# Optimization experiments

Hardware: AMD Instinct MI355X
Metric: run time of the kernel (lower is better)

## Reference

```python
import math
import jax, jax.numpy as jnp
import numpy as np

HEADS = 16
MASKED_BIAS = -10000.0


def setup_inputs() -> dict:
    key = jax.random.key(0)
    kq, kk, kv = jax.random.split(key, 3)
    B, S, D = 4, 1024, 2048
    q = jax.random.normal(kq, (B, S, D), dtype=jnp.float32)
    k = jax.random.normal(kk, (B, S, D), dtype=jnp.float32)
    v = jax.random.normal(kv, (B, S, D), dtype=jnp.float32)
    return {"q": q, "k": k, "v": v}


def _mha(q, k, v):
    B, Sq, D = q.shape
    Sk = k.shape[-2]
    hd = D // HEADS
    # (B, H, S, hd)
    qh = q.reshape(B, Sq, HEADS, hd).transpose(0, 2, 1, 3)
    kh = k.reshape(B, Sk, HEADS, hd).transpose(0, 2, 1, 3)
    vh = v.reshape(B, Sk, HEADS, hd).transpose(0, 2, 1, 3)
    scores = jnp.einsum("bhqd,bhkd->bhqk", qh, kh) / math.sqrt(hd)
    # causal mask: query i attends to keys <= i (aligned to end of kv)
    qi = jnp.arange(Sq)[:, None] + (Sk - Sq)
    ki = jnp.arange(Sk)[None, :]
    causal = ki <= qi  # (Sq, Sk)
    scores = jnp.where(causal[None, None], scores, jnp.asarray(MASKED_BIAS, scores.dtype))
    attn = jax.nn.softmax(scores, axis=-1)
    out = jnp.einsum("bhqk,bhkd->bhqd", attn, vh)
    return out.transpose(0, 2, 1, 3).reshape(B, Sq, D)


def reference(q, k, v):
    return _mha(q, k, v)
```

## Files before the change

### kernel.cpp

```cpp
#include <hip/hip_runtime.h>
#include <hip/hip_bf16.h>


#define HEADS  16
#define HD     128
#define SEQ    1024
#define DMODEL 2048

typedef _Float16 f16;
typedef __attribute__((ext_vector_type(8))) _Float16 f16x8;
typedef __attribute__((ext_vector_type(4))) _Float16 f16x4;
typedef __attribute__((ext_vector_type(4))) float    f32x4;
typedef __attribute__((ext_vector_type(4))) unsigned int u32x4;

__device__ __forceinline__ unsigned int pkrtz(float a, float b) {
    return __builtin_bit_cast(unsigned int, __builtin_amdgcn_cvt_pkrtz(a, b));
}

__global__ __launch_bounds__(256, 2)
void fa_fwd(const float* __restrict__ Q,
            const float* __restrict__ K,
            const float* __restrict__ V,
            float* __restrict__ O)
{
    __shared__ f16 kT[2][64 * 128];
    __shared__ f16 vT[2][128 * 64];

    const int tid  = threadIdx.x;
    const int lane = tid & 63;
    const int wv   = tid >> 6;
    const int quad = lane >> 4;
    const int cl   = lane & 15;

    const int bh = blockIdx.x;
    const int qt = 15 - blockIdx.y;
    const int qb = qt * 64;
    const long long head_off = ((long long)(bh >> 4) * SEQ) * DMODEL
                             + (long long)(bh & 15) * HD;
    const float rscale = 0.08838834764831845f;

    const int krow = tid >> 4;
    const int kg   = tid & 15;
    const int kgs  = kg ^ krow;
    const int vr0  = (tid & 31) * 2;
    const int vcg  = tid >> 5;
    const int vg   = vr0 >> 3;
    const int vo   = vr0 & 7;

    f32x4 kraw[8], vraw[8];

    auto loadKV = [&](int kbase) {
        #pragma unroll
        for (int i = 0; i < 4; ++i) {
            const float* kp = K + head_off + (long long)(kbase + krow + i * 16) * DMODEL + kg * 8;
            kraw[2 * i]     = *(const f32x4*)kp;
            kraw[2 * i + 1] = *(const f32x4*)(kp + 4);
        }
        const float* vp = V + head_off + (long long)(kbase + vr0) * DMODEL + vcg * 16;
        #pragma unroll
        for (int j = 0; j < 4; ++j) {
            vraw[j]     = *(const f32x4*)(vp + 4 * j);
            vraw[4 + j] = *(const f32x4*)(vp + DMODEL + 4 * j);
        }
    };

    auto stageKV = [&](int buf) {
        #pragma unroll
        for (int i = 0; i < 4; ++i) {
            u32x4 w;
            w.x = pkrtz(kraw[2 * i][0], kraw[2 * i][1]);
            w.y = pkrtz(kraw[2 * i][2], kraw[2 * i][3]);
            w.z = pkrtz(kraw[2 * i + 1][0], kraw[2 * i + 1][1]);
            w.w = pkrtz(kraw[2 * i + 1][2], kraw[2 * i + 1][3]);
            *(u32x4*)&kT[buf][(krow + 16 * i) * 128 + kgs * 8] = w;
        }
        #pragma unroll
        for (int j = 0; j < 16; ++j) {
            unsigned int pk = pkrtz(vraw[j >> 2][j & 3], vraw[4 + (j >> 2)][j & 3]);
            *(unsigned int*)&vT[buf][(vcg * 16 + j) * 64 + ((vg ^ (j & 7)) * 8) + vo] = pk;
        }
    };

    const int qrow = qb + wv * 16 + cl;
    f16x8 qf[4];
    {
        const float* qp = Q + head_off + (long long)qrow * DMODEL + quad * 8;
        #pragma unroll
        for (int kk = 0; kk < 4; ++kk) {
            f32x4 qa = *(const f32x4*)(qp + kk * 32);
            f32x4 qc = *(const f32x4*)(qp + kk * 32 + 4);
            union { f16x8 v; unsigned int u[4]; } qw;
            qw.u[0] = pkrtz(qa[0], qa[1]);
            qw.u[1] = pkrtz(qa[2], qa[3]);
            qw.u[2] = pkrtz(qc[0], qc[1]);
            qw.u[3] = pkrtz(qc[2], qc[3]);
            qf[kk] = qw.v;
        }
    }

    f32x4 acc[8];
    #pragma unroll
    for (int i = 0; i < 8; ++i) acc[i] = (f32x4){0.f, 0.f, 0.f, 0.f};
    float ls = 0.f;

    loadKV(0);
    stageKV(0);
    __syncthreads();

    #pragma unroll 1
    for (int kt = 0; kt <= qt; ++kt) {
        const int c = kt & 1;

        if (kt < qt) loadKV((kt + 1) * 64);

        f32x4 sc[4];
        #pragma unroll
        for (int st = 0; st < 4; ++st) sc[st] = (f32x4){0.f, 0.f, 0.f, 0.f};
        __builtin_amdgcn_s_setprio(1);
        #pragma unroll
        for (int kk = 0; kk < 4; ++kk) {
            #pragma unroll
            for (int st = 0; st < 4; ++st) {
                f16x8 kf = *(const f16x8*)&kT[c][(st * 16 + cl) * 128
                                               + ((kk * 4 + quad) ^ cl) * 8];
                sc[st] = __builtin_amdgcn_mfma_f32_16x16x32_f16(kf, qf[kk], sc[st], 0, 0, 0);
            }
        }
        __builtin_amdgcn_s_setprio(0);

        if (kt < qt) stageKV(c ^ 1);

        const int kbase = kt * 64;
        f16x4 pf[4];
        if (kt == qt) {
            #pragma unroll
            for (int st = 0; st < 4; ++st) {
                float e[4];
                #pragma unroll
                for (int r = 0; r < 4; ++r) {
                    int key = kbase + st * 16 + quad * 4 + r;
                    float ex = __expf(sc[st][r] * rscale);
                    e[r] = (key <= qrow) ? ex : 0.f;
                    ls += e[r];
                }
                union { f16x4 v; unsigned int u[2]; } pw;
                pw.u[0] = pkrtz(e[0], e[1]);
                pw.u[1] = pkrtz(e[2], e[3]);
                pf[st] = pw.v;
            }
        } else {
            #pragma unroll
            for (int st = 0; st < 4; ++st) {
                float e[4];
                #pragma unroll
                for (int r = 0; r < 4; ++r) {
                    e[r] = __expf(sc[st][r] * rscale);
                    ls += e[r];
                }
                union { f16x4 v; unsigned int u[2]; } pw;
                pw.u[0] = pkrtz(e[0], e[1]);
                pw.u[1] = pkrtz(e[2], e[3]);
                pf[st] = pw.v;
            }
        }

        __builtin_amdgcn_s_setprio(1);
        #pragma unroll
        for (int dt = 0; dt < 8; ++dt) {
            #pragma unroll
            for (int st = 0; st < 4; ++st) {
                f16x4 vf = *(const f16x4*)&vT[c][(dt * 16 + cl) * 64
                                                + ((st * 2 + (quad >> 1)) ^ (cl & 7)) * 8
                                                + (quad & 1) * 4];
                acc[dt] = __builtin_amdgcn_mfma_f32_16x16x16f16(vf, pf[st], acc[dt], 0, 0, 0);
            }
        }
        __builtin_amdgcn_s_setprio(0);

        if (kt < qt) __syncthreads();
    }

    float lsum = ls;
    lsum += __shfl_xor(lsum, 16, 64);
    lsum += __shfl_xor(lsum, 32, 64);
    const float rl = 1.0f / lsum;

    float* op = O + head_off + (long long)qrow * DMODEL + quad * 4;
    #pragma unroll
    for (int dt = 0; dt < 8; ++dt) {
        f32x4 o4 = acc[dt];
        o4[0] *= rl; o4[1] *= rl; o4[2] *= rl; o4[3] *= rl;
        *(f32x4*)(op + dt * 16) = o4;
    }
}

extern "C" void kernel_launch(void* const* d_in, const int* in_sizes, int n_in,
                              void* d_out, int out_size, void* d_ws, size_t ws_size,
                              hipStream_t stream) {
    const float* q = (const float*)d_in[0];
    const float* k = (const float*)d_in[1];
    const float* v = (const float*)d_in[2];
    float* o = (float*)d_out;

    dim3 grid(4 * HEADS, SEQ / 64);
    dim3 block(256);
    fa_fwd<<<grid, block, 0, stream>>>(q, k, v, o);
}
```

Baseline: 170.5 us.

## Pre-convert K/V to swizzled fp16 image and DMA tiles directly into LDS

Adds a prep kernel that converts each 64-key K/V tile from fp32 to fp16 in the attention kernel's swizzled LDS layout and stores it in a global scratch image. The attention kernel then fills LDS with global_load_lds DMA copies instead of loading fp32 into registers, converting and storing to LDS on every reuse. This aims to halve the global bytes re-read per tile and free registers and ALU work in the main loop. The trade-off is an extra kernel launch, an extra pass over K/V, and reliance on the barrier to wait for the asynchronous LDS DMA to complete.

```diff
diff --git a/kernel.cpp b/kernel.cpp
--- a/kernel.cpp
+++ b/kernel.cpp
@@ -6,6 +6,7 @@
 #define HD     128
 #define SEQ    1024
 #define DMODEL 2048
+#define IMG_CHUNK 32768
 
 typedef _Float16 f16;
 typedef __attribute__((ext_vector_type(8))) _Float16 f16x8;
@@ -13,15 +14,77 @@
 typedef __attribute__((ext_vector_type(4))) float    f32x4;
 typedef __attribute__((ext_vector_type(4))) unsigned int u32x4;
 
+typedef __attribute__((address_space(1))) const unsigned char gl_u8;
+typedef __attribute__((address_space(3))) unsigned char lds_u8;
+
+__device__ unsigned char KVIMG[64ull * 16ull * IMG_CHUNK];
+
 __device__ __forceinline__ unsigned int pkrtz(float a, float b) {
     return __builtin_bit_cast(unsigned int, __builtin_amdgcn_cvt_pkrtz(a, b));
 }
 
+__device__ __forceinline__ void dma16(const void* g, void* l) {
+    __builtin_amdgcn_global_load_lds((gl_u8*)g, (lds_u8*)l, 16, 0, 0);
+}
+
 __global__ __launch_bounds__(256, 2)
-void fa_fwd(const float* __restrict__ Q,
-            const float* __restrict__ K,
-            const float* __restrict__ V,
-            float* __restrict__ O)
+void prep_kv(const float* __restrict__ K, const float* __restrict__ V)
+{
+    __shared__ f16 kL[64 * 128];
+    __shared__ f16 vL[128 * 64];
+
+    const int tid = threadIdx.x;
+    const int bh  = blockIdx.x;
+    const int kb  = blockIdx.y;
+    const long long head_off = ((long long)(bh >> 4) * SEQ) * DMODEL
+                             + (long long)(bh & 15) * HD;
+    const int kbase = kb * 64;
+
+    const int krow = tid >> 4;
+    const int kg   = tid & 15;
+    const int kgs  = kg ^ krow;
+    #pragma unroll
+    for (int i = 0; i < 4; ++i) {
+        const float* kp = K + head_off + (long long)(kbase + krow + 16 * i) * DMODEL + kg * 8;
+        f32x4 a = *(const f32x4*)kp;
+        f32x4 b = *(const f32x4*)(kp + 4);
+        u32x4 w;
+        w.x = pkrtz(a[0], a[1]); w.y = pkrtz(a[2], a[3]);
+        w.z = pkrtz(b[0], b[1]); w.w = pkrtz(b[2], b[3]);
+        *(u32x4*)&kL[(krow + 16 * i) * 128 + kgs * 8] = w;
+    }
+    const int vr0 = (tid & 31) * 2;
+    const int vcg = tid >> 5;
+    const int vg  = vr0 >> 3;
+    const int vo  = vr0 & 7;
+    {
+        const float* vp = V + head_off + (long long)(kbase + vr0) * DMODEL + vcg * 16;
+        f32x4 va[4], vb[4];
+        #pragma unroll
+        for (int j = 0; j < 4; ++j) {
+            va[j] = *(const f32x4*)(vp + 4 * j);
+            vb[j] = *(const f32x4*)(vp + DMODEL + 4 * j);
+        }
+        #pragma unroll
+        for (int j = 0; j < 16; ++j) {
+            unsigned int pk = pkrtz(va[j >> 2][j & 3], vb[j >> 2][j & 3]);
+            *(unsigned int*)&vL[(vcg * 16 + j) * 64 + ((vg ^ (j & 7)) * 8) + vo] = pk;
+        }
+    }
+    __syncthreads();
+
+    unsigned char* dst = KVIMG + ((long long)(bh * 16 + kb)) * IMG_CHUNK;
+    const unsigned char* ks = (const unsigned char*)kL;
+    const unsigned char* vs = (const unsigned char*)vL;
+    #pragma unroll
+    for (int i = 0; i < 4; ++i) {
+        *(u32x4*)(dst + tid * 16 + i * 4096)         = *(const u32x4*)(ks + tid * 16 + i * 4096);
+        *(u32x4*)(dst + 16384 + tid * 16 + i * 4096) = *(const u32x4*)(vs + tid * 16 + i * 4096);
+    }
+}
+
+__global__ __launch_bounds__(256, 2)
+void fa_fwd(const float* __restrict__ Q, float* __restrict__ O)
 {
     __shared__ f16 kT[2][64 * 128];
     __shared__ f16 vT[2][128 * 64];
@@ -39,46 +102,16 @@
                              + (long long)(bh & 15) * HD;
     const float rscale = 0.08838834764831845f;
 
-    const int krow = tid >> 4;
-    const int kg   = tid & 15;
-    const int kgs  = kg ^ krow;
-    const int vr0  = (tid & 31) * 2;
-    const int vcg  = tid >> 5;
-    const int vg   = vr0 >> 3;
-    const int vo   = vr0 & 7;
-
-    f32x4 kraw[8], vraw[8];
-
-    auto loadKV = [&](int kbase) {
-        #pragma unroll
-        for (int i = 0; i < 4; ++i) {
-            const float* kp = K + head_off + (long long)(kbase + krow + i * 16) * DMODEL + kg * 8;
-            kraw[2 * i]     = *(const f32x4*)kp;
-            kraw[2 * i + 1] = *(const f32x4*)(kp + 4);
-        }
-        const float* vp = V + head_off + (long long)(kbase + vr0) * DMODEL + vcg * 16;
-        #pragma unroll
-        for (int j = 0; j < 4; ++j) {
-            vraw[j]     = *(const f32x4*)(vp + 4 * j);
-            vraw[4 + j] = *(const f32x4*)(vp + DMODEL + 4 * j);
-        }
-    };
-
-    auto stageKV = [&](int buf) {
-        #pragma unroll
-        for (int i = 0; i < 4; ++i) {
-            u32x4 w;
-            w.x = pkrtz(kraw[2 * i][0], kraw[2 * i][1]);
-            w.y = pkrtz(kraw[2 * i][2], kraw[2 * i][3]);
-            w.z = pkrtz(kraw[2 * i + 1][0], kraw[2 * i + 1][1]);
-            w.w = pkrtz(kraw[2 * i + 1][2], kraw[2 * i + 1][3]);
-            *(u32x4*)&kT[buf][(krow + 16 * i) * 128 + kgs * 8] = w;
-        }
-        #pragma unroll
-        for (int j = 0; j < 16; ++j) {
-            unsigned int pk = pkrtz(vraw[j >> 2][j & 3], vraw[4 + (j >> 2)][j & 3]);
-            *(unsigned int*)&vT[buf][(vcg * 16 + j) * 64 + ((vg ^ (j & 7)) * 8) + vo] = pk;
-        }
+    const unsigned char* img = KVIMG + (long long)bh * 16 * IMG_CHUNK;
+
+    auto issueTile = [&](int buf, int kt) {
+        const unsigned char* src = img + (long long)kt * IMG_CHUNK + wv * 4096 + lane * 16;
+        unsigned char* kb = (unsigned char*)&kT[buf][0] + wv * 4096;
+        unsigned char* vb = (unsigned char*)&vT[buf][0] + wv * 4096;
+        #pragma unroll
+        for (int i = 0; i < 4; ++i) dma16(src + i * 1024,          kb + i * 1024);
+        #pragma unroll
+        for (int i = 0; i < 4; ++i) dma16(src + 16384 + i * 1024,  vb + i * 1024);
     };
 
     const int qrow = qb + wv * 16 + cl;
@@ -103,15 +136,15 @@
     for (int i = 0; i < 8; ++i) acc[i] = (f32x4){0.f, 0.f, 0.f, 0.f};
     float ls = 0.f;
 
-    loadKV(0);
-    stageKV(0);
-    __syncthreads();
+    issueTile(0, 0);
 
     #pragma unroll 1
     for (int kt = 0; kt <= qt; ++kt) {
         const int c = kt & 1;
 
-        if (kt < qt) loadKV((kt + 1) * 64);
+        __syncthreads();
+
+        if (kt < qt) issueTile(c ^ 1, kt + 1);
 
         f32x4 sc[4];
         #pragma unroll
@@ -127,8 +160,6 @@
             }
         }
         __builtin_amdgcn_s_setprio(0);
-
-        if (kt < qt) stageKV(c ^ 1);
 
         const int kbase = kt * 64;
         f16x4 pf[4];
@@ -176,8 +207,6 @@
             }
         }
         __builtin_amdgcn_s_setprio(0);
-
-        if (kt < qt) __syncthreads();
     }
 
     float lsum = ls;
@@ -202,7 +231,6 @@
     const float* v = (const float*)d_in[2];
     float* o = (float*)d_out;
 
-    dim3 grid(4 * HEADS, SEQ / 64);
-    dim3 block(256);
-    fa_fwd<<<grid, block, 0, stream>>>(q, k, v, o);
-}
+    prep_kv<<<dim3(64, 16), dim3(256), 0, stream>>>(k, v);
+    fa_fwd <<<dim3(64, 16), dim3(256), 0, stream>>>(q, o);
+}
```

Result: slower. 174.2 us (+2.2%).
